# Optimization experiments

Hardware: AMD Instinct MI355X
Metric: run time of the kernel (lower is better)

## Reference

```python
import jax, jax.numpy as jnp
import numpy as np

EPS = 1e-5  # matches repo calc_mean_std eps


def _mvn(x):
    # mean-variance normalization per (B, C) over spatial dims, unbiased var (torch default)
    B, C, H, W = x.shape
    xf = x.reshape(B, C, H * W)
    m = xf.mean(-1, keepdims=True)
    v = xf.var(-1, ddof=1, keepdims=True)
    return ((xf - m) / jnp.sqrt(v + EPS)).reshape(x.shape)


def _conv1x1(x, w, b):
    # 1x1 conv == per-pixel channel mixing
    return jnp.einsum('oc,bchw->bohw', w, x) + b[None, :, None, None]


def _content_sa(x, Wp, bp):
    B, C, H, W = x.shape
    n = H * W
    xn = _mvn(x)
    q = _conv1x1(xn, Wp[0], bp[0]).reshape(B, C, n)  # f
    k = _conv1x1(xn, Wp[1], bp[1]).reshape(B, C, n)  # g
    energy = jnp.einsum('bci,bcj->bij', q, k)        # [B, N, N]
    attn = jax.nn.softmax(energy, axis=-1)
    v = _conv1x1(x, Wp[2], bp[2]).reshape(B, C, n)   # h
    out = jnp.einsum('bcj,bij->bci', v, attn).reshape(B, C, H, W)
    return _conv1x1(out, Wp[3], bp[3]) + x


def _style_sa(x, Wp, bp):
    B, C, H, W = x.shape
    n = H * W
    f = _conv1x1(x, Wp[0], bp[0]).reshape(B, C, n)
    g = _conv1x1(x, Wp[1], bp[1]).reshape(B, C, n)
    energy = jnp.einsum('bci,bdi->bcd', f, g)        # [B, C, C] channel attention
    attn = jax.nn.softmax(energy, axis=-1)
    h = _conv1x1(_mvn(x), Wp[2], bp[2]).reshape(B, C, n)
    out = jnp.einsum('bdc,bdi->bci', attn, h).reshape(B, C, H, W)  # attn^T @ h
    return _conv1x1(out, Wp[3], bp[3]) + x


def _ca(c, s, Wp, bp):
    B, C, Hc, Wc = c.shape
    nc = Hc * Wc
    _, _, Hs, Ws = s.shape
    ns = Hs * Ws
    q = _conv1x1(_mvn(c), Wp[0], bp[0]).reshape(B, C, nc)
    k = _conv1x1(_mvn(s), Wp[1], bp[1]).reshape(B, C, ns)
    energy = jnp.einsum('bci,bcj->bij', q, k)        # [B, Nc, Ns]
    attn = jax.nn.softmax(energy, axis=-1)
    v = _conv1x1(s, Wp[2], bp[2]).reshape(B, C, ns)
    out = jnp.einsum('bcj,bij->bci', v, attn).reshape(B, C, Hc, Wc)
    return _conv1x1(out, Wp[3], bp[3]) + c


def setup_inputs() -> dict:
    key = jax.random.key(0)
    ks = jax.random.split(key, 8)
    B, C, H, W = 4, 512, 64, 64
    scale = 0.02
    return {
        'content_feat': jax.random.normal(ks[0], (B, C, H, W), jnp.float32),
        'style_feat': jax.random.normal(ks[1], (B, C, H, W), jnp.float32),
        'csa_w': jax.random.normal(ks[2], (4, C, C), jnp.float32) * scale,
        'csa_b': jnp.zeros((4, C), jnp.float32),
        'ssa_w': jax.random.normal(ks[3], (4, C, C), jnp.float32) * scale,
        'ssa_b': jnp.zeros((4, C), jnp.float32),
        'ca_w': jax.random.normal(ks[4], (4, C, C), jnp.float32) * scale,
        'ca_b': jnp.zeros((4, C), jnp.float32),
    }


def reference(content_feat, style_feat, csa_w, csa_b, ssa_w, ssa_b, ca_w, ca_b):
    cf = _content_sa(content_feat, csa_w, csa_b)
    sf = _style_sa(style_feat, ssa_w, ssa_b)
    return _ca(cf, sf, ca_w, ca_b)
```

## Files before the change

kernel.cpp:

```cpp
#include <hip/hip_runtime.h>
#include <math.h>


#define B_ 4
#define C_ 512
#define N_ 4096
#define TM 128
#define TN 128

typedef unsigned short u16;
typedef __attribute__((ext_vector_type(8))) short s8v;
typedef __attribute__((ext_vector_type(4))) float f4v;

__device__ __forceinline__ u16 f2bf(float x) {
  unsigned u = __float_as_uint(x);
  return (u16)((u + 0x7fffu + ((u >> 16) & 1u)) >> 16);
}
__device__ __forceinline__ u16 f2h(float x) {
  union { _Float16 h; u16 u; } z;
  z.h = (_Float16)x;
  return z.u;
}
__device__ __forceinline__ float h2f(u16 v) {
  union { _Float16 h; u16 u; } z;
  z.u = v;
  return (float)z.h;
}

__device__ __forceinline__ void gload16(const void* g, void* l) {
  __builtin_amdgcn_global_load_lds(
      (const __attribute__((address_space(1))) unsigned int*)g,
      (__attribute__((address_space(3))) unsigned int*)l, 16, 0, 0);
}

__device__ __forceinline__ float wave_red_sum(float v) {
#pragma unroll
  for (int off = 32; off > 0; off >>= 1) v += __shfl_xor(v, off, 64);
  return v;
}
__device__ __forceinline__ float wave_red_max(float v) {
#pragma unroll
  for (int off = 32; off > 0; off >>= 1) v = fmaxf(v, __shfl_xor(v, off, 64));
  return v;
}

__global__ __launch_bounds__(256) void row_stats_k(const float* __restrict__ x,
                                                   float* __restrict__ mean,
                                                   float* __restrict__ rstd) {
  long row = blockIdx.x;
  const float* p = x + row * (long)N_;
  int t = threadIdx.x;
  float s = 0.f, ss = 0.f;
  for (int i = t * 4; i < N_; i += 1024) {
    float4 v = *(const float4*)(p + i);
    s += v.x + v.y + v.z + v.w;
    ss += v.x * v.x + v.y * v.y + v.z * v.z + v.w * v.w;
  }
  __shared__ float rs_[4], rss_[4];
  int wid = t >> 6, lane = t & 63;
  s = wave_red_sum(s);
  ss = wave_red_sum(ss);
  if (lane == 0) { rs_[wid] = s; rss_[wid] = ss; }
  __syncthreads();
  if (t == 0) {
    float S = rs_[0] + rs_[1] + rs_[2] + rs_[3];
    float SS = rss_[0] + rss_[1] + rss_[2] + rss_[3];
    float m = S / (float)N_;
    float var = (SS - (float)N_ * m * m) / (float)(N_ - 1);
    mean[row] = m;
    rstd[row] = rsqrtf(var + 1e-5f);
  }
}

__global__ __launch_bounds__(256) void cvt3_k(
    const float* __restrict__ a, const float* __restrict__ b,
    const float* __restrict__ c, u16* __restrict__ oa, u16* __restrict__ ob,
    u16* __restrict__ oc, long n) {
  const float* in = blockIdx.y == 0 ? a : (blockIdx.y == 1 ? b : c);
  u16* o = blockIdx.y == 0 ? oa : (blockIdx.y == 1 ? ob : oc);
  long i = ((long)blockIdx.x * 256 + threadIdx.x) * 4;
  if (i >= n) return;
  float4 v = *(const float4*)(in + i);
  *(ushort4*)(o + i) = make_ushort4(f2bf(v.x), f2bf(v.y), f2bf(v.z), f2bf(v.w));
}

template <bool HAS2>
__global__ __launch_bounds__(256) void t_cvt_k(
    const float* __restrict__ X, const float* __restrict__ mean,
    const float* __restrict__ rstd, u16* __restrict__ o1,
    u16* __restrict__ o2) {
  __shared__ float tile[64][68];
  const int b = blockIdx.z;
  const int c0 = blockIdx.y * 64, i0 = blockIdx.x * 64;
  const int t = threadIdx.x;
  const int tr = t >> 4, tc = (t & 15) << 2;
  const long CN = (long)C_ * N_;
  const float* Xb = X + (long)b * CN;
#pragma unroll
  for (int p2 = 0; p2 < 4; ++p2) {
    int c = p2 * 16 + tr;
    float4 v = *(const float4*)(Xb + (long)(c0 + c) * N_ + i0 + tc);
    tile[c][tc] = v.x;
    tile[c][tc + 1] = v.y;
    tile[c][tc + 2] = v.z;
    tile[c][tc + 3] = v.w;
  }
  __syncthreads();
  float mv[4], rv[4];
#pragma unroll
  for (int j = 0; j < 4; ++j) {
    mv[j] = mean[b * C_ + c0 + tc + j];
    rv[j] = rstd[b * C_ + c0 + tc + j];
  }
#pragma unroll
  for (int p2 = 0; p2 < 4; ++p2) {
    int ir = p2 * 16 + tr;
    long off = (long)b * CN + (long)(i0 + ir) * C_ + c0 + tc;
    u16 h1[4], h2[4];
#pragma unroll
    for (int j = 0; j < 4; ++j) {
      float v = tile[tc + j][ir];
      if (HAS2) h2[j] = f2bf(v);
      h1[j] = f2bf((v - mv[j]) * rv[j]);
    }
    *(ushort4*)(o1 + off) = make_ushort4(h1[0], h1[1], h1[2], h1[3]);
    if (HAS2) *(ushort4*)(o2 + off) = make_ushort4(h2[0], h2[1], h2[2], h2[3]);
  }
}

__global__ __launch_bounds__(256) void softmax_bf_k(const u16* __restrict__ E,
                                                    u16* __restrict__ ph) {
  long row = blockIdx.x;
  const u16* p = E + row * (long)N_;
  int t = threadIdx.x;
  float v[16];
  float mx = -3.4e38f;
#pragma unroll
  for (int q = 0; q < 4; ++q) {
    ushort4 w4 = *(const ushort4*)(p + t * 16 + q * 4);
    v[q * 4 + 0] = h2f(w4.x);
    v[q * 4 + 1] = h2f(w4.y);
    v[q * 4 + 2] = h2f(w4.z);
    v[q * 4 + 3] = h2f(w4.w);
    mx = fmaxf(mx, fmaxf(fmaxf(v[q * 4], v[q * 4 + 1]),
                         fmaxf(v[q * 4 + 2], v[q * 4 + 3])));
  }
  __shared__ float red[4];
  int wid = t >> 6, lane = t & 63;
  mx = wave_red_max(mx);
  if (lane == 0) red[wid] = mx;
  __syncthreads();
  mx = fmaxf(fmaxf(red[0], red[1]), fmaxf(red[2], red[3]));
  float s = 0.f;
#pragma unroll
  for (int i = 0; i < 16; ++i) {
    v[i] = __expf(v[i] - mx);
    s += v[i];
  }
  __syncthreads();
  s = wave_red_sum(s);
  if (lane == 0) red[wid] = s;
  __syncthreads();
  s = red[0] + red[1] + red[2] + red[3];
  float inv = 1.f / s;
  long ob = row * (long)N_ + t * 16;
#pragma unroll
  for (int q = 0; q < 4; ++q) {
    *(ushort4*)(ph + ob + q * 4) =
        make_ushort4(f2bf(v[q * 4 + 0] * inv), f2bf(v[q * 4 + 1] * inv),
                     f2bf(v[q * 4 + 2] * inv), f2bf(v[q * 4 + 3] * inv));
  }
}

__global__ __launch_bounds__(256) void softmax_t_k(const float* __restrict__ E2,
                                                   u16* __restrict__ ph) {
  int b = blockIdx.x >> 9;
  int x = blockIdx.x & 511;
  const float* p = E2 + ((long)b * C_ + x) * C_;
  int t = threadIdx.x;
  float v0 = p[t * 2], v1 = p[t * 2 + 1];
  float mx = fmaxf(v0, v1);
  __shared__ float red[4];
  int wid = t >> 6, lane = t & 63;
  mx = wave_red_max(mx);
  if (lane == 0) red[wid] = mx;
  __syncthreads();
  mx = fmaxf(fmaxf(red[0], red[1]), fmaxf(red[2], red[3]));
  v0 = __expf(v0 - mx);
  v1 = __expf(v1 - mx);
  float s = v0 + v1;
  __syncthreads();
  s = wave_red_sum(s);
  if (lane == 0) red[wid] = s;
  __syncthreads();
  s = red[0] + red[1] + red[2] + red[3];
  float inv = 1.f / s;
  long base = (long)b * C_ * C_;
  ph[base + (long)(t * 2) * C_ + x] = f2bf(v0 * inv);
  ph[base + (long)(t * 2 + 1) * C_ + x] = f2bf(v1 * inv);
}

__global__ __launch_bounds__(256) void redk_k(const float* __restrict__ P,
                                              long pKS, long perB, int nsplit,
                                              float* __restrict__ of,
                                              long total) {
  long e = ((long)blockIdx.x * 256 + threadIdx.x) * 4;
  if (e >= total) return;
  long b = e / perB, rem = e - b * perB;
  const float* p0 = P + b * perB + rem;
  float4 s = *(const float4*)p0;
  for (int k = 1; k < nsplit; ++k) {
    float4 t = *(const float4*)(p0 + (long)k * pKS);
    s.x += t.x;
    s.y += t.y;
    s.z += t.z;
    s.w += t.w;
  }
  *(float4*)(of + b * perB + rem) = s;
}

template <int OUTM, int BIAS, bool RES>
__global__ __launch_bounds__(256, 3) void mm_k(
    const u16* __restrict__ Ap, long aBS, int lda,
    const u16* __restrict__ Bp, long bBS, int ldb,
    float* Of, u16* __restrict__ Obf, long oBS, long oKS, int ldo,
    const float* __restrict__ bias, const float* resp, long rBS,
    int K, int nsplit) {
  __shared__ u16 lds[16384];
  const int b = blockIdx.z / nsplit;
  const int ks = blockIdx.z % nsplit;
  const int Kc = K / nsplit;
  const int k0beg = ks * Kc;
  const int m0 = blockIdx.y * TM, n0 = blockIdx.x * TN;
  const int t = threadIdx.x, lane = t & 63, wid = t >> 6;
  const int wm = (wid >> 1) * 64, wn = (wid & 1) * 64;

  const u16* srcp = (wid < 2) ? (Ap + (long)b * aBS) : (Bp + (long)b * bBS);
  const int sld = (wid < 2) ? lda : ldb;
  const long srow0 = ((wid < 2) ? m0 : n0) + (wid & 1) * 64;
  u16* dstb = &lds[wid * 4096];
  const int srg = lane >> 3;
  const int ssl = lane & 7;

  f4v acc[4][4];
#pragma unroll
  for (int i = 0; i < 4; ++i)
#pragma unroll
    for (int j = 0; j < 4; ++j) acc[i][j] = (f4v){0.f, 0.f, 0.f, 0.f};

  const int lr = lane & 15, ksl = lane >> 4;
  const u16* lA = &lds[0];
  const u16* lB = &lds[8192];

  for (int k0 = k0beg; k0 < k0beg + Kc; k0 += 64) {
#pragma unroll
    for (int s = 0; s < 8; ++s) {
      int r = s * 8 + srg;
      int kb = ((ssl ^ (r & 7)) << 4);
      const u16* gp = srcp + (srow0 + r) * (long)sld + k0;
      gload16((const char*)gp + kb, dstb + s * 512);
    }
    __syncthreads();
#pragma unroll
    for (int kk = 0; kk < 2; ++kk) {
      s8v ar[4], br[4];
#pragma unroll
      for (int f = 0; f < 4; ++f) {
        int ra = wm + f * 16 + lr;
        ar[f] = *(const s8v*)(lA + ra * 64 +
                              ((((kk << 2) | ksl) ^ (ra & 7)) << 3));
        int rb = wn + f * 16 + lr;
        br[f] = *(const s8v*)(lB + rb * 64 +
                              ((((kk << 2) | ksl) ^ (rb & 7)) << 3));
      }
#pragma unroll
      for (int i = 0; i < 4; ++i)
#pragma unroll
        for (int j = 0; j < 4; ++j)
          acc[i][j] = __builtin_amdgcn_mfma_f32_16x16x32_bf16(
              ar[i], br[j], acc[i][j], 0, 0, 0);
    }
    __syncthreads();
  }

  const float* resb = RES ? (resp + (long)b * rBS) : nullptr;
  long obase = (long)b * oBS + (long)ks * oKS;
#pragma unroll
  for (int i = 0; i < 4; ++i) {
#pragma unroll
    for (int j = 0; j < 4; ++j) {
#pragma unroll
      for (int e = 0; e < 4; ++e) {
        int m = m0 + wm + i * 16 + ksl * 4 + e;
        int n = n0 + wn + j * 16 + lr;
        float v = acc[i][j][e];
        if (BIAS == 1) v += bias[m];
        if (BIAS == 2) v += bias[n];
        long o = obase + (long)m * ldo + n;
        if (OUTM == 0) {
          if (RES) v += resb[(long)m * ldo + n];
          Of[o] = v;
        } else if (OUTM == 1) {
          Obf[o] = f2bf(v);
        } else {
          Obf[o] = f2h(v);
        }
      }
    }
  }
}

extern "C" void kernel_launch(void* const* d_in, const int* in_sizes, int n_in,
                              void* d_out, int out_size, void* d_ws,
                              size_t ws_size, hipStream_t stream) {
  (void)in_sizes; (void)n_in; (void)out_size;
  const long CN = (long)C_ * N_;
  const long CC = (long)C_ * C_;

  const float* xc = (const float*)d_in[0];
  const float* xs = (const float*)d_in[1];
  const float* cw = (const float*)d_in[2];
  const float* cb = (const float*)d_in[3];
  const float* sw = (const float*)d_in[4];
  const float* sb = (const float*)d_in[5];
  const float* aw = (const float*)d_in[6];
  const float* ab = (const float*)d_in[7];
  float* out = (float*)d_out;

  char* w = (char*)d_ws;
  auto carve = [&](size_t bytes) {
    char* r = w;
    w += (bytes + 255) & ~(size_t)255;
    return r;
  };
  u16* cwb = (u16*)carve(4 * CC * 2);
  u16* swb = (u16*)carve(4 * CC * 2);
  u16* awb = (u16*)carve(4 * CC * 2);
  float* stats = (float*)carve(8 * B_ * C_ * 4);
  float* m1 = stats, *r1 = m1 + B_ * C_, *m2 = r1 + B_ * C_, *r2 = m2 + B_ * C_;
  float* m3 = r2 + B_ * C_, *r3 = m3 + B_ * C_, *m4 = r3 + B_ * C_,
       *r4 = m4 + B_ * C_;
  float* E2buf = (float*)carve(B_ * CC * 4);
  u16* aT = (u16*)carve(B_ * CC * 2);
  const size_t SLOT = (size_t)B_ * CN * 4;
  char* s0 = carve(SLOT);
  char* s1 = carve(SLOT);
  char* s2 = carve(SLOT);
  char* s3 = carve(SLOT);
  size_t used = (size_t)(w - (char*)d_ws);
  int S = N_;
  while (S > 128 && used + (size_t)4 * B_ * S * N_ > ws_size) S >>= 1;
  u16* Ereg16 = (u16*)carve((size_t)B_ * S * N_ * 2);
  u16* atB = (u16*)carve((size_t)B_ * S * N_ * 2);
  float* EregF = (float*)Ereg16;

  u16* sA = (u16*)s0;
  u16* sB = (u16*)s1;
  u16* sC = (u16*)s2;
  u16* sD = (u16*)s3;

  const int e2s = 8;

  dim3 blk(256);
  dim3 gQ(4, 32, B_);
  dim3 gV(32, 4, B_);
  dim3 gQK(8, 32, B_);
  dim3 gFG(32, 8, B_);
  dim3 gTs(N_ / 64, C_ / 64, B_);

  cvt3_k<<<dim3(1024, 3), blk, 0, stream>>>(cw, sw, aw, cwb, swb, awb, 4 * CC);

  auto attention = [&](const u16* Qp, int ldq, long qBS, const u16* Kp,
                       int ldk, long kBS, const u16* Vp, u16* oT) {
    for (int i0 = 0; i0 < N_; i0 += S) {
      mm_k<2, 0, false><<<dim3(N_ / TN, S / TM, B_), blk, 0, stream>>>(
          Qp + (long)i0 * ldq, qBS, ldq, Kp, kBS, ldk, nullptr, Ereg16,
          (long)S * N_, 0, N_, nullptr, nullptr, 0, C_, 1);
      softmax_bf_k<<<B_ * S, blk, 0, stream>>>(Ereg16, atB);
      mm_k<1, 0, false><<<dim3(C_ / TN, S / TM, B_), blk, 0, stream>>>(
          atB, (long)S * N_, N_, Vp, CN, N_, nullptr, oT + (long)i0 * C_, CN,
          0, C_, nullptr, nullptr, 0, N_, 1);
    }
  };

  row_stats_k<<<B_ * C_, blk, 0, stream>>>(xc, m1, r1);
  row_stats_k<<<B_ * C_, blk, 0, stream>>>(xs, m2, r2);
  t_cvt_k<true><<<gTs, blk, 0, stream>>>(xc, m1, r1, sA, sB);
  mm_k<1, 2, false><<<gQK, blk, 0, stream>>>(sA, CN, C_, cwb, 0, C_, nullptr,
      sC, (long)N_ * 1024, 0, 1024, cb, nullptr, 0, C_, 1);
  mm_k<1, 1, false><<<gV, blk, 0, stream>>>(cwb + 2 * CC, 0, C_, sB, CN, C_,
      nullptr, sD, CN, 0, N_, cb + 2 * C_, nullptr, 0, C_, 1);
  attention(sC, 1024, (long)N_ * 1024, sC + 512, 1024, (long)N_ * 1024, sD,
            sA);
  mm_k<0, 1, true><<<gV, blk, 0, stream>>>(cwb + 3 * CC, 0, C_, sA, CN, C_,
      out, nullptr, CN, 0, N_, cb + 3 * C_, xc, CN, C_, 1);

  t_cvt_k<true><<<gTs, blk, 0, stream>>>(xs, m2, r2, sA, sC);
  mm_k<1, 1, false><<<gFG, blk, 0, stream>>>(swb, 0, C_, sC, CN, C_, nullptr,
      sD, (long)1024 * N_, 0, N_, sb, nullptr, 0, C_, 1);
  mm_k<1, 2, false><<<gQ, blk, 0, stream>>>(sA, CN, C_, swb + 2 * CC, 0, C_,
      nullptr, sB, CN, 0, C_, sb + 2 * C_, nullptr, 0, C_, 1);
  mm_k<0, 0, false><<<dim3(4, 4, B_ * e2s), blk, 0, stream>>>(
      sD, (long)1024 * N_, N_, sD + (long)512 * N_, (long)1024 * N_, N_,
      EregF, nullptr, CC, (long)B_ * CC, C_, nullptr, nullptr, 0, N_, e2s);
  redk_k<<<(B_ * (int)CC) / 1024, blk, 0, stream>>>(
      EregF, (long)B_ * CC, CC, e2s, E2buf, (long)B_ * CC);
  softmax_t_k<<<B_ * C_, blk, 0, stream>>>(E2buf, aT);
  mm_k<1, 0, false><<<gQ, blk, 0, stream>>>(sB, CN, C_, aT, CC, C_, nullptr,
      sA, CN, 0, C_, nullptr, nullptr, 0, C_, 1);
  float* sfF = (float*)s1;
  mm_k<0, 1, true><<<gV, blk, 0, stream>>>(swb + 3 * CC, 0, C_, sA, CN, C_,
      sfF, nullptr, CN, 0, N_, sb + 3 * C_, xs, CN, C_, 1);

  row_stats_k<<<B_ * C_, blk, 0, stream>>>(out, m3, r3);
  row_stats_k<<<B_ * C_, blk, 0, stream>>>(sfF, m4, r4);
  t_cvt_k<false><<<gTs, blk, 0, stream>>>(out, m3, r3, sC, nullptr);
  t_cvt_k<true><<<gTs, blk, 0, stream>>>(sfF, m4, r4, sD, sA);
  mm_k<1, 2, false><<<gQ, blk, 0, stream>>>(sC, CN, C_, awb, 0, C_, nullptr,
      sB, CN, 0, C_, ab, nullptr, 0, C_, 1);
  mm_k<1, 2, false><<<gQ, blk, 0, stream>>>(sD, CN, C_, awb + CC, 0, C_,
      nullptr, sC, CN, 0, C_, ab + C_, nullptr, 0, C_, 1);
  mm_k<1, 1, false><<<gV, blk, 0, stream>>>(awb + 2 * CC, 0, C_, sA, CN, C_,
      nullptr, sD, CN, 0, N_, ab + 2 * C_, nullptr, 0, C_, 1);
  attention(sB, C_, CN, sC, C_, CN, sD, sA);
  mm_k<0, 1, true><<<gV, blk, 0, stream>>>(awb + 3 * CC, 0, C_, sA, CN, C_,
      out, nullptr, CN, 0, N_, ab + 3 * C_, out, CN, C_, 1);
}
```

Before: 1.139 ms.

## Store intermediate SA outputs in bf16 and rebuild buffer plan for cross-attention

The content and style self-attention outputs (cf, sf) are now written as bf16 instead of fp32. New bf16-input row-stats and transpose-convert kernels read them, and the final residual add reads bf16 through a new residual mode in the matmul epilogue. This halves the memory traffic for these intermediates and frees the fp32 slots, at the cost of rounding the residual and the normalization inputs to bf16. Workspace buffers are reassigned so the attention scratch area also holds transposed operands.

```diff
diff --git a/kernel.cpp b/kernel.cpp
--- a/kernel.cpp
+++ b/kernel.cpp
@@ -15,6 +15,9 @@
 __device__ __forceinline__ u16 f2bf(float x) {
   unsigned u = __float_as_uint(x);
   return (u16)((u + 0x7fffu + ((u >> 16) & 1u)) >> 16);
+}
+__device__ __forceinline__ float bf2f(u16 h) {
+  return __uint_as_float(((unsigned)h) << 16);
 }
 __device__ __forceinline__ u16 f2h(float x) {
   union { _Float16 h; u16 u; } z;
@@ -55,6 +58,38 @@
     float4 v = *(const float4*)(p + i);
     s += v.x + v.y + v.z + v.w;
     ss += v.x * v.x + v.y * v.y + v.z * v.z + v.w * v.w;
+  }
+  __shared__ float rs_[4], rss_[4];
+  int wid = t >> 6, lane = t & 63;
+  s = wave_red_sum(s);
+  ss = wave_red_sum(ss);
+  if (lane == 0) { rs_[wid] = s; rss_[wid] = ss; }
+  __syncthreads();
+  if (t == 0) {
+    float S = rs_[0] + rs_[1] + rs_[2] + rs_[3];
+    float SS = rss_[0] + rss_[1] + rss_[2] + rss_[3];
+    float m = S / (float)N_;
+    float var = (SS - (float)N_ * m * m) / (float)(N_ - 1);
+    mean[row] = m;
+    rstd[row] = rsqrtf(var + 1e-5f);
+  }
+}
+
+__global__ __launch_bounds__(256) void row_stats_bf_k(
+    const u16* __restrict__ x, float* __restrict__ mean,
+    float* __restrict__ rstd) {
+  long row = blockIdx.x;
+  const u16* p = x + row * (long)N_;
+  int t = threadIdx.x;
+  float s = 0.f, ss = 0.f;
+  for (int i = t * 8; i < N_; i += 2048) {
+    ushort4 a = *(const ushort4*)(p + i);
+    ushort4 b = *(const ushort4*)(p + i + 4);
+    float v0 = bf2f(a.x), v1 = bf2f(a.y), v2 = bf2f(a.z), v3 = bf2f(a.w);
+    float v4 = bf2f(b.x), v5 = bf2f(b.y), v6 = bf2f(b.z), v7 = bf2f(b.w);
+    s += v0 + v1 + v2 + v3 + v4 + v5 + v6 + v7;
+    ss += v0 * v0 + v1 * v1 + v2 * v2 + v3 * v3 + v4 * v4 + v5 * v5 +
+          v6 * v6 + v7 * v7;
   }
   __shared__ float rs_[4], rss_[4];
   int wid = t >> 6, lane = t & 63;
@@ -104,6 +139,50 @@
     tile[c][tc + 1] = v.y;
     tile[c][tc + 2] = v.z;
     tile[c][tc + 3] = v.w;
+  }
+  __syncthreads();
+  float mv[4], rv[4];
+#pragma unroll
+  for (int j = 0; j < 4; ++j) {
+    mv[j] = mean[b * C_ + c0 + tc + j];
+    rv[j] = rstd[b * C_ + c0 + tc + j];
+  }
+#pragma unroll
+  for (int p2 = 0; p2 < 4; ++p2) {
+    int ir = p2 * 16 + tr;
+    long off = (long)b * CN + (long)(i0 + ir) * C_ + c0 + tc;
+    u16 h1[4], h2[4];
+#pragma unroll
+    for (int j = 0; j < 4; ++j) {
+      float v = tile[tc + j][ir];
+      if (HAS2) h2[j] = f2bf(v);
+      h1[j] = f2bf((v - mv[j]) * rv[j]);
+    }
+    *(ushort4*)(o1 + off) = make_ushort4(h1[0], h1[1], h1[2], h1[3]);
+    if (HAS2) *(ushort4*)(o2 + off) = make_ushort4(h2[0], h2[1], h2[2], h2[3]);
+  }
+}
+
+template <bool HAS2>
+__global__ __launch_bounds__(256) void t_cvt_bf_k(
+    const u16* __restrict__ X, const float* __restrict__ mean,
+    const float* __restrict__ rstd, u16* __restrict__ o1,
+    u16* __restrict__ o2) {
+  __shared__ float tile[64][68];
+  const int b = blockIdx.z;
+  const int c0 = blockIdx.y * 64, i0 = blockIdx.x * 64;
+  const int t = threadIdx.x;
+  const int tr = t >> 4, tc = (t & 15) << 2;
+  const long CN = (long)C_ * N_;
+  const u16* Xb = X + (long)b * CN;
+#pragma unroll
+  for (int p2 = 0; p2 < 4; ++p2) {
+    int c = p2 * 16 + tr;
+    ushort4 v = *(const ushort4*)(Xb + (long)(c0 + c) * N_ + i0 + tc);
+    tile[c][tc] = bf2f(v.x);
+    tile[c][tc + 1] = bf2f(v.y);
+    tile[c][tc + 2] = bf2f(v.z);
+    tile[c][tc + 3] = bf2f(v.w);
   }
   __syncthreads();
   float mv[4], rv[4];
@@ -219,13 +298,13 @@
   *(float4*)(of + b * perB + rem) = s;
 }
 
-template <int OUTM, int BIAS, bool RES>
+template <int OUTM, int BIAS, int RESM>
 __global__ __launch_bounds__(256, 3) void mm_k(
     const u16* __restrict__ Ap, long aBS, int lda,
     const u16* __restrict__ Bp, long bBS, int ldb,
     float* Of, u16* __restrict__ Obf, long oBS, long oKS, int ldo,
-    const float* __restrict__ bias, const float* resp, long rBS,
-    int K, int nsplit) {
+    const float* __restrict__ bias, const float* resp,
+    const u16* __restrict__ res16, long rBS, int K, int nsplit) {
   __shared__ u16 lds[16384];
   const int b = blockIdx.z / nsplit;
   const int ks = blockIdx.z % nsplit;
@@ -283,7 +362,8 @@
     __syncthreads();
   }
 
-  const float* resb = RES ? (resp + (long)b * rBS) : nullptr;
+  const float* resb = (RESM == 1) ? (resp + (long)b * rBS) : nullptr;
+  const u16* resb16 = (RESM == 2) ? (res16 + (long)b * rBS) : nullptr;
   long obase = (long)b * oBS + (long)ks * oKS;
 #pragma unroll
   for (int i = 0; i < 4; ++i) {
@@ -296,9 +376,10 @@
         float v = acc[i][j][e];
         if (BIAS == 1) v += bias[m];
         if (BIAS == 2) v += bias[n];
+        if (RESM == 1) v += resb[(long)m * ldo + n];
+        if (RESM == 2) v += bf2f(resb16[(long)m * ldo + n]);
         long o = obase + (long)m * ldo + n;
         if (OUTM == 0) {
-          if (RES) v += resb[(long)m * ldo + n];
           Of[o] = v;
         } else if (OUTM == 1) {
           Obf[o] = f2bf(v);
@@ -350,14 +431,17 @@
   size_t used = (size_t)(w - (char*)d_ws);
   int S = N_;
   while (S > 128 && used + (size_t)4 * B_ * S * N_ > ws_size) S >>= 1;
-  u16* Ereg16 = (u16*)carve((size_t)B_ * S * N_ * 2);
-  u16* atB = (u16*)carve((size_t)B_ * S * N_ * 2);
-  float* EregF = (float*)Ereg16;
+  u16* E16 = (u16*)carve((size_t)B_ * S * N_ * 2);
+  u16* AT = (u16*)carve((size_t)B_ * S * N_ * 2);
+  float* EregF = (float*)E16;
 
   u16* sA = (u16*)s0;
   u16* sB = (u16*)s1;
   u16* sC = (u16*)s2;
   u16* sD = (u16*)s3;
+  u16* at0 = AT;
+  u16* at1 = AT + B_ * CN;
+  u16* at2 = AT + 2 * B_ * CN;
 
   const int e2s = 8;
 
@@ -373,56 +457,56 @@
   auto attention = [&](const u16* Qp, int ldq, long qBS, const u16* Kp,
                        int ldk, long kBS, const u16* Vp, u16* oT) {
     for (int i0 = 0; i0 < N_; i0 += S) {
-      mm_k<2, 0, false><<<dim3(N_ / TN, S / TM, B_), blk, 0, stream>>>(
-          Qp + (long)i0 * ldq, qBS, ldq, Kp, kBS, ldk, nullptr, Ereg16,
-          (long)S * N_, 0, N_, nullptr, nullptr, 0, C_, 1);
-      softmax_bf_k<<<B_ * S, blk, 0, stream>>>(Ereg16, atB);
-      mm_k<1, 0, false><<<dim3(C_ / TN, S / TM, B_), blk, 0, stream>>>(
-          atB, (long)S * N_, N_, Vp, CN, N_, nullptr, oT + (long)i0 * C_, CN,
-          0, C_, nullptr, nullptr, 0, N_, 1);
+      mm_k<2, 0, 0><<<dim3(N_ / TN, S / TM, B_), blk, 0, stream>>>(
+          Qp + (long)i0 * ldq, qBS, ldq, Kp, kBS, ldk, nullptr, E16,
+          (long)S * N_, 0, N_, nullptr, nullptr, nullptr, 0, C_, 1);
+      softmax_bf_k<<<B_ * S, blk, 0, stream>>>(E16, AT);
+      mm_k<1, 0, 0><<<dim3(C_ / TN, S / TM, B_), blk, 0, stream>>>(
+          AT, (long)S * N_, N_, Vp, CN, N_, nullptr, oT + (long)i0 * C_, CN,
+          0, C_, nullptr, nullptr, nullptr, 0, N_, 1);
     }
   };
 
   row_stats_k<<<B_ * C_, blk, 0, stream>>>(xc, m1, r1);
   row_stats_k<<<B_ * C_, blk, 0, stream>>>(xs, m2, r2);
   t_cvt_k<true><<<gTs, blk, 0, stream>>>(xc, m1, r1, sA, sB);
-  mm_k<1, 2, false><<<gQK, blk, 0, stream>>>(sA, CN, C_, cwb, 0, C_, nullptr,
-      sC, (long)N_ * 1024, 0, 1024, cb, nullptr, 0, C_, 1);
-  mm_k<1, 1, false><<<gV, blk, 0, stream>>>(cwb + 2 * CC, 0, C_, sB, CN, C_,
-      nullptr, sD, CN, 0, N_, cb + 2 * C_, nullptr, 0, C_, 1);
+  mm_k<1, 2, 0><<<gQK, blk, 0, stream>>>(sA, CN, C_, cwb, 0, C_, nullptr, sC,
+      (long)N_ * 1024, 0, 1024, cb, nullptr, nullptr, 0, C_, 1);
+  mm_k<1, 1, 0><<<gV, blk, 0, stream>>>(cwb + 2 * CC, 0, C_, sB, CN, C_,
+      nullptr, sD, CN, 0, N_, cb + 2 * C_, nullptr, nullptr, 0, C_, 1);
   attention(sC, 1024, (long)N_ * 1024, sC + 512, 1024, (long)N_ * 1024, sD,
             sA);
-  mm_k<0, 1, true><<<gV, blk, 0, stream>>>(cwb + 3 * CC, 0, C_, sA, CN, C_,
-      out, nullptr, CN, 0, N_, cb + 3 * C_, xc, CN, C_, 1);
+  mm_k<1, 1, 1><<<gV, blk, 0, stream>>>(cwb + 3 * CC, 0, C_, sA, CN, C_,
+      nullptr, sB, CN, 0, N_, cb + 3 * C_, xc, nullptr, CN, C_, 1);
 
   t_cvt_k<true><<<gTs, blk, 0, stream>>>(xs, m2, r2, sA, sC);
-  mm_k<1, 1, false><<<gFG, blk, 0, stream>>>(swb, 0, C_, sC, CN, C_, nullptr,
-      sD, (long)1024 * N_, 0, N_, sb, nullptr, 0, C_, 1);
-  mm_k<1, 2, false><<<gQ, blk, 0, stream>>>(sA, CN, C_, swb + 2 * CC, 0, C_,
-      nullptr, sB, CN, 0, C_, sb + 2 * C_, nullptr, 0, C_, 1);
-  mm_k<0, 0, false><<<dim3(4, 4, B_ * e2s), blk, 0, stream>>>(
+  mm_k<1, 1, 0><<<gFG, blk, 0, stream>>>(swb, 0, C_, sC, CN, C_, nullptr, sD,
+      (long)1024 * N_, 0, N_, sb, nullptr, nullptr, 0, C_, 1);
+  mm_k<1, 2, 0><<<gQ, blk, 0, stream>>>(sA, CN, C_, swb + 2 * CC, 0, C_,
+      nullptr, at0, CN, 0, C_, sb + 2 * C_, nullptr, nullptr, 0, C_, 1);
+  mm_k<0, 0, 0><<<dim3(4, 4, B_ * e2s), blk, 0, stream>>>(
       sD, (long)1024 * N_, N_, sD + (long)512 * N_, (long)1024 * N_, N_,
-      EregF, nullptr, CC, (long)B_ * CC, C_, nullptr, nullptr, 0, N_, e2s);
+      EregF, nullptr, CC, (long)B_ * CC, C_, nullptr, nullptr, nullptr, 0, N_,
+      e2s);
   redk_k<<<(B_ * (int)CC) / 1024, blk, 0, stream>>>(
       EregF, (long)B_ * CC, CC, e2s, E2buf, (long)B_ * CC);
   softmax_t_k<<<B_ * C_, blk, 0, stream>>>(E2buf, aT);
-  mm_k<1, 0, false><<<gQ, blk, 0, stream>>>(sB, CN, C_, aT, CC, C_, nullptr,
-      sA, CN, 0, C_, nullptr, nullptr, 0, C_, 1);
-  float* sfF = (float*)s1;
-  mm_k<0, 1, true><<<gV, blk, 0, stream>>>(swb + 3 * CC, 0, C_, sA, CN, C_,
-      sfF, nullptr, CN, 0, N_, sb + 3 * C_, xs, CN, C_, 1);
-
-  row_stats_k<<<B_ * C_, blk, 0, stream>>>(out, m3, r3);
-  row_stats_k<<<B_ * C_, blk, 0, stream>>>(sfF, m4, r4);
-  t_cvt_k<false><<<gTs, blk, 0, stream>>>(out, m3, r3, sC, nullptr);
-  t_cvt_k<true><<<gTs, blk, 0, stream>>>(sfF, m4, r4, sD, sA);
-  mm_k<1, 2, false><<<gQ, blk, 0, stream>>>(sC, CN, C_, awb, 0, C_, nullptr,
-      sB, CN, 0, C_, ab, nullptr, 0, C_, 1);
-  mm_k<1, 2, false><<<gQ, blk, 0, stream>>>(sD, CN, C_, awb + CC, 0, C_,
-      nullptr, sC, CN, 0, C_, ab + C_, nullptr, 0, C_, 1);
-  mm_k<1, 1, false><<<gV, blk, 0, stream>>>(awb + 2 * CC, 0, C_, sA, CN, C_,
-      nullptr, sD, CN, 0, N_, ab + 2 * C_, nullptr, 0, C_, 1);
-  attention(sB, C_, CN, sC, C_, CN, sD, sA);
-  mm_k<0, 1, true><<<gV, blk, 0, stream>>>(awb + 3 * CC, 0, C_, sA, CN, C_,
-      out, nullptr, CN, 0, N_, ab + 3 * C_, out, CN, C_, 1);
-}
+  mm_k<1, 0, 0><<<gQ, blk, 0, stream>>>(at0, CN, C_, aT, CC, C_, nullptr, sA,
+      CN, 0, C_, nullptr, nullptr, nullptr, 0, C_, 1);
+  mm_k<1, 1, 1><<<gV, blk, 0, stream>>>(swb + 3 * CC, 0, C_, sA, CN, C_,
+      nullptr, sC, CN, 0, N_, sb + 3 * C_, xs, nullptr, CN, C_, 1);
+
+  row_stats_bf_k<<<B_ * C_, blk, 0, stream>>>(sB, m3, r3);
+  row_stats_bf_k<<<B_ * C_, blk, 0, stream>>>(sC, m4, r4);
+  t_cvt_bf_k<false><<<gTs, blk, 0, stream>>>(sB, m3, r3, at0, nullptr);
+  t_cvt_bf_k<true><<<gTs, blk, 0, stream>>>(sC, m4, r4, at1, at2);
+  mm_k<1, 2, 0><<<gQ, blk, 0, stream>>>(at0, CN, C_, awb, 0, C_, nullptr, sD,
+      CN, 0, C_, ab, nullptr, nullptr, 0, C_, 1);
+  mm_k<1, 2, 0><<<gQ, blk, 0, stream>>>(at1, CN, C_, awb + CC, 0, C_, nullptr,
+      sA, CN, 0, C_, ab + C_, nullptr, nullptr, 0, C_, 1);
+  mm_k<1, 1, 0><<<gV, blk, 0, stream>>>(awb + 2 * CC, 0, C_, at2, CN, C_,
+      nullptr, sC, CN, 0, N_, ab + 2 * C_, nullptr, nullptr, 0, C_, 1);
+  attention(sD, C_, CN, sA, C_, CN, sC, sD);
+  mm_k<0, 1, 2><<<gV, blk, 0, stream>>>(awb + 3 * CC, 0, C_, sD, CN, C_, out,
+      nullptr, CN, 0, N_, ab + 3 * C_, nullptr, sB, CN, C_, 1);
+}
```

Result: faster. 1.085 ms (-4.7%).
